# Performance work log

Hardware: AMD Instinct MI355X
Metric: run time of the kernel (lower is better)

Reference implementation:

```python
import jax, jax.numpy as jnp
import numpy as np

DIM = 192
D_STATE = 16
D_CONV = 4
EXPAND = 2
D_INNER = DIM * EXPAND          # 384
DT_RANK = (DIM + 15) // 16      # 12
B_SZ, H_SP, W_SP = 4, 64, 64


def setup_inputs() -> dict:
    key = jax.random.key(0)
    ks = jax.random.split(key, 8)
    f = jax.random.normal
    return {
        "x": f(ks[0], (B_SZ, DIM, H_SP, W_SP), jnp.float32),
        "ln_w": jnp.ones((DIM,), jnp.float32),
        "ln_b": jnp.zeros((DIM,), jnp.float32),
        "in_proj_w": f(ks[1], (2 * D_INNER, DIM), jnp.float32) * 0.02,
        "conv_w": f(ks[2], (D_INNER, D_CONV), jnp.float32) * 0.2,
        "conv_b": jnp.zeros((D_INNER,), jnp.float32),
        "x_proj_w": f(ks[3], (DT_RANK + 2 * D_STATE, D_INNER), jnp.float32) * 0.02,
        "dt_proj_w": f(ks[4], (D_INNER, DT_RANK), jnp.float32) * 0.1,
        "dt_proj_b": f(ks[5], (D_INNER,), jnp.float32) * 0.1,
        "A_log": jnp.log(jnp.broadcast_to(
            jnp.arange(1, D_STATE + 1, dtype=jnp.float32), (D_INNER, D_STATE))),
        "D": jnp.ones((D_INNER,), jnp.float32),
        "out_proj_w": f(ks[6], (DIM, D_INNER), jnp.float32) * 0.02,
    }


def _mamba_block(x, ln_w, ln_b, in_proj_w, conv_w, conv_b, x_proj_w,
                 dt_proj_w, dt_proj_b, A_log, D, out_proj_w):
    B, C, H, W = x.shape
    L = H * W
    # [B,C,H,W] -> [B,L,C]
    xf = x.transpose(0, 2, 3, 1).reshape(B, L, C)

    # LayerNorm
    mu = xf.mean(-1, keepdims=True)
    var = ((xf - mu) ** 2).mean(-1, keepdims=True)
    xn = (xf - mu) * jax.lax.rsqrt(var + 1e-5) * ln_w + ln_b

    # in_proj -> xm (ssm branch), z (gate branch)
    xz = xn @ in_proj_w.T                      # [B,L,2*Di]
    xm, z = jnp.split(xz, 2, axis=-1)

    # causal depthwise conv1d over sequence (pad left d_conv-1)
    xc = xm.transpose(0, 2, 1)                 # [B,Di,L]
    xc = jax.lax.conv_general_dilated(
        xc, conv_w[:, None, :], (1,), [(D_CONV - 1, 0)],
        dimension_numbers=("NCH", "OIH", "NCH"),
        feature_group_count=D_INNER)
    xc = xc + conv_b[None, :, None]
    xm = jax.nn.silu(xc.transpose(0, 2, 1))    # [B,L,Di]

    # x_proj -> dt, B, C (input-dependent SSM params)
    dbc = xm @ x_proj_w.T                      # [B,L,dt_rank+2N]
    dt, Bm, Cm = jnp.split(dbc, [DT_RANK, DT_RANK + D_STATE], axis=-1)
    dt = jax.nn.softplus(dt @ dt_proj_w.T + dt_proj_b)  # [B,L,Di]

    A = -jnp.exp(A_log)                        # [Di,N]

    def step(h, inp):
        xt, dtt, Bt, Ct = inp                  # [B,Di],[B,Di],[B,N],[B,N]
        dA = jnp.exp(dtt[..., None] * A)       # [B,Di,N]
        h = h * dA + (dtt * xt)[..., None] * Bt[:, None, :]
        y = jnp.einsum('bdn,bn->bd', h, Ct)
        return h, y

    h0 = jnp.zeros((B, D_INNER, D_STATE), xm.dtype)
    scan_in = (xm.transpose(1, 0, 2), dt.transpose(1, 0, 2),
               Bm.transpose(1, 0, 2), Cm.transpose(1, 0, 2))
    _, ys = jax.lax.scan(step, h0, scan_in)    # [L,B,Di]

    y = ys.transpose(1, 0, 2) + xm * D         # skip term D*x
    y = y * jax.nn.silu(z)                     # gate
    out = y @ out_proj_w.T                     # [B,L,C]

    out = xf + out                             # residual
    return out.reshape(B, H, W, C).transpose(0, 3, 1, 2)


def reference(x, ln_w, ln_b, in_proj_w, conv_w, conv_b, x_proj_w,
              dt_proj_w, dt_proj_b, A_log, D, out_proj_w):
    return _mamba_block(x, ln_w, ln_b, in_proj_w, conv_w, conv_b, x_proj_w,
                        dt_proj_w, dt_proj_b, A_log, D, out_proj_w)
```

## Files before the change

kernel.cpp:

```cpp
#include <hip/hip_runtime.h>
#include <hip/hip_bf16.h>
#include <cstdint>
#include <cmath>

#define DIMC   192
#define DSTATE 16
#define DCONV  4
#define DINNER 384
#define DTRANK 12
#define BSZ    4
#define HSP    64
#define WSP    64
#define LSEQ   4096
#define NTOK   (BSZ*LSEQ)
#define XPN    (DTRANK + 2*DSTATE)
#define XZW    (2*DINNER)
#define LC4    16
#define NCH4   (LSEQ/LC4)
#define NXP    448

typedef unsigned short ushortT;
using short8 = __attribute__((ext_vector_type(8))) short;
using f32x4  = __attribute__((ext_vector_type(4))) float;

__device__ __forceinline__ float bflo(unsigned u) { return __uint_as_float(u << 16); }
__device__ __forceinline__ float bfhi(unsigned u) { return __uint_as_float(u & 0xffff0000u); }
__device__ __forceinline__ float bf2f(ushortT u) { return __uint_as_float(((unsigned)u) << 16); }
__device__ __forceinline__ unsigned pkbf(float lo, float hi) {
  __hip_bfloat16 l = __float2bfloat16(lo), h = __float2bfloat16(hi);
  return (unsigned)*(ushortT*)&l | ((unsigned)*(ushortT*)&h << 16);
}
#define UNPK8(arr, base, v4)                                        \
  arr[base + 0] = bflo(v4.x); arr[base + 1] = bfhi(v4.x);           \
  arr[base + 2] = bflo(v4.y); arr[base + 3] = bfhi(v4.y);           \
  arr[base + 4] = bflo(v4.z); arr[base + 5] = bfhi(v4.z);           \
  arr[base + 6] = bflo(v4.w); arr[base + 7] = bfhi(v4.w);

__global__ __launch_bounds__(256) void wcvt_kernel(
    const float* __restrict__ w_in, const float* __restrict__ w_out,
    __hip_bfloat16* __restrict__ wbf) {
  int gid = blockIdx.x * 256 + threadIdx.x;
  float v = gid < 147456 ? w_in[gid] : w_out[gid - 147456];
  wbf[gid] = __float2bfloat16(v);
}

__global__ __launch_bounds__(256) void wcomb_kernel(
    const float* __restrict__ xpw, const float* __restrict__ dtw,
    __hip_bfloat16* __restrict__ wcb) {
  int gid = blockIdx.x * 256 + threadIdx.x;
  int dd = gid / 384, k = gid % 384;
  float v = 0.f;
  if (dd < 384) {
#pragma unroll
    for (int j = 0; j < 12; ++j) v = fmaf(dtw[dd * 12 + j], xpw[j * 384 + k], v);
  } else if (dd < 416) {
    v = xpw[(dd - 372) * 384 + k];
  }
  wcb[gid] = __float2bfloat16(v);
}

__global__ __launch_bounds__(512) void ln_kernel(
    const float* __restrict__ x, const float* __restrict__ ln_w,
    const float* __restrict__ ln_b, __hip_bfloat16* __restrict__ xn) {
  __shared__ float xs[DIMC][WSP + 1];
  __shared__ float mu_s[WSP], rs_s[WSP];
  int bh = blockIdx.x;
  int b = bh >> 6, h = bh & 63;
  int tid = threadIdx.x;
  const float* xb = x + (size_t)b * DIMC * LSEQ + (size_t)h * WSP;
  for (int e = tid; e < DIMC * WSP; e += 512) {
    int c = e >> 6, w = e & 63;
    xs[c][w] = xb[(size_t)c * LSEQ + w];
  }
  __syncthreads();
  {
    int w = tid >> 3, p = tid & 7;
    float s = 0.f, s2 = 0.f;
#pragma unroll
    for (int i = 0; i < 24; ++i) {
      float v = xs[p * 24 + i][w];
      s += v; s2 = fmaf(v, v, s2);
    }
    s  += __shfl_xor(s, 1);  s2 += __shfl_xor(s2, 1);
    s  += __shfl_xor(s, 2);  s2 += __shfl_xor(s2, 2);
    s  += __shfl_xor(s, 4);  s2 += __shfl_xor(s2, 4);
    if (p == 0) {
      float mu = s * (1.f / DIMC);
      float var = s2 * (1.f / DIMC) - mu * mu;
      mu_s[w] = mu;
      rs_s[w] = rsqrtf(var + 1e-5f);
    }
  }
  __syncthreads();
  __hip_bfloat16* xo = xn + (size_t)(b * LSEQ + h * WSP) * DIMC;
  for (int e = tid; e < DIMC * WSP; e += 512) {
    int w = e / DIMC, c = e % DIMC;
    xo[(size_t)w * DIMC + c] =
        __float2bfloat16((xs[c][w] - mu_s[w]) * rs_s[w] * ln_w[c] + ln_b[c]);
  }
}

template<int WM, int WN, int FM, int FN, int EPI>
__global__ __launch_bounds__(256) void gemm_bf16(
    const ushortT* __restrict__ A, const ushortT* __restrict__ B,
    void* __restrict__ Cv, void* __restrict__ Cv2,
    const ushortT* __restrict__ xm_aux, const float* __restrict__ bias384,
    const float* __restrict__ xres, int K, int Nreal, int ldc) {
  constexpr int BM = WM * FM * 16, BN = WN * FN * 16;
  __shared__ ushortT As[BM][72];
  __shared__ ushortT Bs[BN][72];
  int bm = blockIdx.x * BM, bn = blockIdx.y * BN;
  int tid = threadIdx.x, lane = tid & 63, w = tid >> 6;
  int wm = w / WN, wn = w % WN;
  int lm = lane & 15, lk = lane >> 4;
  const ushortT* Bb = B;
  size_t zoff = 0;
  if constexpr (EPI == 1) {
    size_t zb = blockIdx.z;
    Bb = B + zb * (size_t)LSEQ * K;
    zoff = zb * (size_t)DIMC * LSEQ;
  }
  f32x4 acc[FM][FN];
#pragma unroll
  for (int mi = 0; mi < FM; ++mi)
#pragma unroll
    for (int ni = 0; ni < FN; ++ni) acc[mi][ni] = (f32x4){0.f, 0.f, 0.f, 0.f};

  for (int k0 = 0; k0 < K; k0 += 64) {
    __syncthreads();
    for (int v = tid; v < BM * 8; v += 256) {
      int row = v >> 3, c8 = v & 7;
      *(uint4*)&As[row][c8 * 8] =
          *(const uint4*)(A + (size_t)(bm + row) * K + k0 + c8 * 8);
    }
    for (int v = tid; v < BN * 8; v += 256) {
      int row = v >> 3, c8 = v & 7;
      *(uint4*)&Bs[row][c8 * 8] =
          *(const uint4*)(Bb + (size_t)(bn + row) * K + k0 + c8 * 8);
    }
    __syncthreads();
#pragma unroll
    for (int ks = 0; ks < 2; ++ks) {
      short8 af[FM], bfr[FN];
#pragma unroll
      for (int mi = 0; mi < FM; ++mi)
        af[mi] = *(const short8*)&As[wm * FM * 16 + mi * 16 + lm][ks * 32 + lk * 8];
#pragma unroll
      for (int ni = 0; ni < FN; ++ni)
        bfr[ni] = *(const short8*)&Bs[wn * FN * 16 + ni * 16 + lm][ks * 32 + lk * 8];
#pragma unroll
      for (int mi = 0; mi < FM; ++mi)
#pragma unroll
        for (int ni = 0; ni < FN; ++ni)
          acc[mi][ni] = __builtin_amdgcn_mfma_f32_16x16x32_bf16(
              af[mi], bfr[ni], acc[mi][ni], 0, 0, 0);
    }
  }
#pragma unroll
  for (int mi = 0; mi < FM; ++mi) {
#pragma unroll
    for (int ni = 0; ni < FN; ++ni) {
      int ncol = bn + wn * FN * 16 + ni * 16 + lm;
#pragma unroll
      for (int r = 0; r < 4; ++r) {
        int m = bm + wm * FM * 16 + mi * 16 + lk * 4 + r;
        if constexpr (EPI == 1) {
          size_t aidx = zoff + (size_t)m * LSEQ + ncol;
          ((float*)Cv)[aidx] = xres[aidx] + acc[mi][ni][r];
        } else if constexpr (EPI == 2) {
          if (ncol < Nreal)
            ((__hip_bfloat16*)Cv)[(size_t)m * ldc + ncol] =
                __float2bfloat16(acc[mi][ni][r]);
        } else {
          if (ncol < 384) {
            float dtr = acc[mi][ni][r] + bias384[ncol];
            float dt = dtr > 15.f ? dtr : __logf(1.f + __expf(dtr));
            float xmv = bf2f(xm_aux[(size_t)m * DINNER + ncol]);
            ((unsigned*)Cv)[(size_t)m * DINNER + ncol] = pkbf(dt, xmv);
          } else if (ncol < 416) {
            __hip_bfloat16 bv = __float2bfloat16(acc[mi][ni][r]);
            ((ushortT*)Cv2)[(size_t)m * 48 + 16 + (ncol - 384)] = *(ushortT*)&bv;
          }
        }
      }
    }
  }
}

__global__ __launch_bounds__(256) void conv_silu_kernel(
    const __hip_bfloat16* __restrict__ xz, const float* __restrict__ conv_w,
    const float* __restrict__ conv_b, __hip_bfloat16* __restrict__ xmh) {
  int g8 = blockIdx.x * 256 + threadIdx.x;
  int d8 = g8 % 48;
  int tok = g8 / 48;
  int l = tok & (LSEQ - 1);
  int d0 = d8 * 8;
  const ushortT* base = (const ushortT*)xz + (size_t)tok * XZW + d0;
  uint4 r0, r1, r2, r3;
  r3 = *(const uint4*)(base);
  r2 = l >= 1 ? *(const uint4*)(base - XZW)     : (uint4){0, 0, 0, 0};
  r1 = l >= 2 ? *(const uint4*)(base - 2 * XZW) : (uint4){0, 0, 0, 0};
  r0 = l >= 3 ? *(const uint4*)(base - 3 * XZW) : (uint4){0, 0, 0, 0};
  float x0[8], x1[8], x2[8], x3[8];
  UNPK8(x0, 0, r0) UNPK8(x1, 0, r1) UNPK8(x2, 0, r2) UNPK8(x3, 0, r3)
  ushortT outv[8];
#pragma unroll
  for (int j = 0; j < 8; ++j) {
    const float4 w = *(const float4*)(conv_w + (d0 + j) * 4);
    float acc = conv_b[d0 + j];
    acc = fmaf(w.x, x0[j], acc);
    acc = fmaf(w.y, x1[j], acc);
    acc = fmaf(w.z, x2[j], acc);
    acc = fmaf(w.w, x3[j], acc);
    float s = acc / (1.f + __expf(-acc));
    __hip_bfloat16 sb = __float2bfloat16(s);
    outv[j] = *(ushortT*)&sb;
  }
  *(uint4*)((ushortT*)xmh + (size_t)tok * DINNER + d0) = *(uint4*)outv;
}

__global__ __launch_bounds__(384) void scan_part1(
    const unsigned* __restrict__ dxpk, const ushortT* __restrict__ dbc,
    const float* __restrict__ A_log, unsigned* __restrict__ hpk) {
  __shared__ ushortT dbc_s[16 * 48];
  int d = threadIdx.x, c = blockIdx.x, b = blockIdx.y;
  size_t rowbase = (size_t)b * LSEQ + (size_t)c * LC4;
  if (d < 96) {
    int row = d / 6, q = d % 6;
    ((uint4*)dbc_s)[d] = ((const uint4*)(dbc + (rowbase + row) * 48))[q];
  }
  float Ac2[16];
#pragma unroll
  for (int q = 0; q < 4; ++q) {
    float4 t4 = *(const float4*)(A_log + d * 16 + q * 4);
    Ac2[q * 4 + 0] = -__expf(t4.x) * 1.44269504f;
    Ac2[q * 4 + 1] = -__expf(t4.y) * 1.44269504f;
    Ac2[q * 4 + 2] = -__expf(t4.z) * 1.44269504f;
    Ac2[q * 4 + 3] = -__expf(t4.w) * 1.44269504f;
  }
  float h[16];
#pragma unroll
  for (int n = 0; n < 16; ++n) h[n] = 0.f;
  float sdt = 0.f;
  const unsigned* pkp = dxpk + rowbase * DINNER + d;
  __syncthreads();
#pragma unroll
  for (int t0 = 0; t0 < 16; t0 += 4) {
    unsigned pk[4];
#pragma unroll
    for (int j = 0; j < 4; ++j) pk[j] = pkp[(t0 + j) * DINNER];
#pragma unroll
    for (int j = 0; j < 4; ++j) {
      int t = t0 + j;
      float dtt = bflo(pk[j]), xmv = bfhi(pk[j]);
      sdt += dtt;
      float dx = dtt * xmv;
      const char* bb = (const char*)dbc_s + t * 96;
      uint4 B0 = *(const uint4*)(bb + 32);
      uint4 B1 = *(const uint4*)(bb + 48);
      float Bv[16];
      UNPK8(Bv, 0, B0)
      UNPK8(Bv, 8, B1)
#pragma unroll
      for (int n = 0; n < 16; ++n) {
        float a = __builtin_amdgcn_exp2f(dtt * Ac2[n]);
        h[n] = fmaf(h[n], a, dx * Bv[n]);
      }
    }
  }
  unsigned up[16];
#pragma unroll
  for (int n = 0; n < 16; ++n)
    up[n] = pkbf(h[n], __builtin_amdgcn_exp2f(Ac2[n] * sdt));
  uint4* hp4 = (uint4*)(hpk + (((size_t)b * NCH4 + c) * DINNER + d) * 16);
#pragma unroll
  for (int q = 0; q < 4; ++q) hp4[q] = *(uint4*)&up[q * 4];
}

__global__ __launch_bounds__(256) void scan_part2(
    const unsigned* __restrict__ hpk, ushortT* __restrict__ hinb) {
  int e = blockIdx.x * 256 + threadIdx.x;
  int b = blockIdx.y;
  float H = 0.f;
  size_t base = (size_t)b * NCH4 * (DINNER * DSTATE) + e;
#pragma unroll 16
  for (int c = 0; c < NCH4; ++c) {
    size_t idx = base + (size_t)c * (DINNER * DSTATE);
    unsigned w = hpk[idx];
    __hip_bfloat16 hb = __float2bfloat16(H);
    hinb[idx] = *(ushortT*)&hb;
    H = fmaf(bfhi(w), H, bflo(w));
  }
}

__global__ __launch_bounds__(384) void scan_part3(
    const unsigned* __restrict__ dxpk, const ushortT* __restrict__ dbc,
    const __hip_bfloat16* __restrict__ xz, const float* __restrict__ A_log,
    const float* __restrict__ Dvec, const ushortT* __restrict__ hinb,
    __hip_bfloat16* __restrict__ ybuf) {
  __shared__ ushortT dbc_s[16 * 48];
  int d = threadIdx.x, c = blockIdx.x, b = blockIdx.y;
  size_t rowbase = (size_t)b * LSEQ + (size_t)c * LC4;
  if (d < 96) {
    int row = d / 6, q = d % 6;
    ((uint4*)dbc_s)[d] = ((const uint4*)(dbc + (rowbase + row) * 48))[q];
  }
  float Ac2[16];
#pragma unroll
  for (int q = 0; q < 4; ++q) {
    float4 t4 = *(const float4*)(A_log + d * 16 + q * 4);
    Ac2[q * 4 + 0] = -__expf(t4.x) * 1.44269504f;
    Ac2[q * 4 + 1] = -__expf(t4.y) * 1.44269504f;
    Ac2[q * 4 + 2] = -__expf(t4.z) * 1.44269504f;
    Ac2[q * 4 + 3] = -__expf(t4.w) * 1.44269504f;
  }
  float h[16];
  {
    const uint4* hp = (const uint4*)(hinb + (((size_t)b * NCH4 + c) * DINNER + d) * 16);
    uint4 h0 = hp[0], h1 = hp[1];
    UNPK8(h, 0, h0)
    UNPK8(h, 8, h1)
  }
  float Dd = Dvec[d];
  const unsigned* pkp = dxpk + rowbase * DINNER + d;
  const ushortT* zp = (const ushortT*)xz + rowbase * XZW + DINNER + d;
  __hip_bfloat16* yp = ybuf + rowbase * DINNER + d;
  __syncthreads();
#pragma unroll
  for (int t0 = 0; t0 < 16; t0 += 4) {
    unsigned pk[4];
    ushortT zv4[4];
#pragma unroll
    for (int j = 0; j < 4; ++j) {
      pk[j] = pkp[(t0 + j) * DINNER];
      zv4[j] = zp[(t0 + j) * XZW];
    }
#pragma unroll
    for (int j = 0; j < 4; ++j) {
      int t = t0 + j;
      float dtt = bflo(pk[j]), xmv = bfhi(pk[j]);
      float dx = dtt * xmv;
      const char* bb = (const char*)dbc_s + t * 96;
      uint4 B0 = *(const uint4*)(bb + 32);
      uint4 B1 = *(const uint4*)(bb + 48);
      uint4 C0 = *(const uint4*)(bb + 64);
      uint4 C1 = *(const uint4*)(bb + 80);
      float Bv[16], Cw[16];
      UNPK8(Bv, 0, B0)
      UNPK8(Bv, 8, B1)
      UNPK8(Cw, 0, C0)
      UNPK8(Cw, 8, C1)
      float y0 = 0.f, y1 = 0.f, y2 = 0.f, y3 = 0.f;
#pragma unroll
      for (int n = 0; n < 16; n += 4) {
        float a0 = __builtin_amdgcn_exp2f(dtt * Ac2[n + 0]);
        float a1 = __builtin_amdgcn_exp2f(dtt * Ac2[n + 1]);
        float a2 = __builtin_amdgcn_exp2f(dtt * Ac2[n + 2]);
        float a3 = __builtin_amdgcn_exp2f(dtt * Ac2[n + 3]);
        h[n + 0] = fmaf(h[n + 0], a0, dx * Bv[n + 0]);
        h[n + 1] = fmaf(h[n + 1], a1, dx * Bv[n + 1]);
        h[n + 2] = fmaf(h[n + 2], a2, dx * Bv[n + 2]);
        h[n + 3] = fmaf(h[n + 3], a3, dx * Bv[n + 3]);
        y0 = fmaf(h[n + 0], Cw[n + 0], y0);
        y1 = fmaf(h[n + 1], Cw[n + 1], y1);
        y2 = fmaf(h[n + 2], Cw[n + 2], y2);
        y3 = fmaf(h[n + 3], Cw[n + 3], y3);
      }
      float yv = fmaf(xmv, Dd, (y0 + y1) + (y2 + y3));
      float zv = bf2f(zv4[j]);
      float gt = zv * __builtin_amdgcn_rcpf(
          1.f + __builtin_amdgcn_exp2f(zv * -1.44269504f));
      yp[(size_t)t * DINNER] = __float2bfloat16(yv * gt);
    }
  }
}

extern "C" void kernel_launch(void* const* d_in, const int* in_sizes, int n_in,
                              void* d_out, int out_size, void* d_ws, size_t ws_size,
                              hipStream_t stream) {
  const float* x        = (const float*)d_in[0];
  const float* ln_w     = (const float*)d_in[1];
  const float* ln_b     = (const float*)d_in[2];
  const float* in_proj  = (const float*)d_in[3];
  const float* conv_w   = (const float*)d_in[4];
  const float* conv_b   = (const float*)d_in[5];
  const float* x_proj   = (const float*)d_in[6];
  const float* dt_w     = (const float*)d_in[7];
  const float* dt_b     = (const float*)d_in[8];
  const float* A_log    = (const float*)d_in[9];
  const float* Dvec     = (const float*)d_in[10];
  const float* out_proj = (const float*)d_in[11];
  float* out = (float*)d_out;

  float* ws = (float*)d_ws;
  __hip_bfloat16* xzb  = (__hip_bfloat16*)ws;
  __hip_bfloat16* xmh  = (__hip_bfloat16*)(ws + 6291456);
  ushortT*        dbcb = (ushortT*)(ws + 9437184);
  unsigned*       dxpk = (unsigned*)(ws + 9830400);
  unsigned*       hpk  = (unsigned*)(ws + 16121856);
  ushortT*        hinb = (ushortT*)(ws + 22413312);
  __hip_bfloat16* ybuf = (__hip_bfloat16*)(ws + 25559040);
  __hip_bfloat16* xnbf = (__hip_bfloat16*)(ws + 28704768);
  __hip_bfloat16* wbf  = (__hip_bfloat16*)(ws + 30277632);
  __hip_bfloat16* wcb  = (__hip_bfloat16*)(ws + 30388224);

  const ushortT* win  = (const ushortT*)wbf;
  const ushortT* wout = (const ushortT*)(wbf + 147456);

  wcvt_kernel<<<864, 256, 0, stream>>>(in_proj, out_proj, wbf);
  wcomb_kernel<<<672, 256, 0, stream>>>(x_proj, dt_w, wcb);

  ln_kernel<<<BSZ * HSP, 512, 0, stream>>>(x, ln_w, ln_b, xnbf);

  gemm_bf16<2, 2, 4, 4, 2><<<dim3(NTOK / 128, XZW / 128), 256, 0, stream>>>(
      (const ushortT*)xnbf, win, xzb, nullptr, nullptr, nullptr, nullptr,
      DIMC, XZW, XZW);

  conv_silu_kernel<<<(NTOK * DINNER / 8) / 256, 256, 0, stream>>>(
      xzb, conv_w, conv_b, xmh);

  gemm_bf16<2, 2, 4, 2, 4><<<dim3(NTOK / 128, NXP / 64), 256, 0, stream>>>(
      (const ushortT*)xmh, (const ushortT*)wcb, dxpk, dbcb,
      (const ushortT*)xmh, dt_b, nullptr, DINNER, NXP, 0);

  scan_part1<<<dim3(NCH4, BSZ), 384, 0, stream>>>(dxpk, dbcb, A_log, hpk);
  scan_part2<<<dim3(DINNER * DSTATE / 256, BSZ), 256, 0, stream>>>(hpk, hinb);
  scan_part3<<<dim3(NCH4, BSZ), 384, 0, stream>>>(
      dxpk, dbcb, xzb, A_log, Dvec, hinb, ybuf);

  gemm_bf16<2, 2, 2, 4, 1><<<dim3(DIMC / 64, LSEQ / 128, BSZ), 256, 0, stream>>>(
      wout, (const ushortT*)ybuf, out, nullptr, nullptr, nullptr, x,
      DINNER, LSEQ, LSEQ);
}
```

Before: 174.7 us.

## Prefetch GEMM tiles in registers, stage out_proj epilogue, merge weight prep kernels

The GEMM now prefetches the next K-slice of A and B into registers while the current tile is being consumed from LDS, so global loads overlap with MFMA work. The out_proj epilogue is staged through LDS (reusing the tile buffer) so the residual read and the output write become coalesced float4 accesses. The two weight-preparation kernels are merged into one launch. The x_proj GEMM is padded to 512 columns and retiled to 128-wide blocks. The padding computes extra zero columns in exchange for fewer, larger blocks, and the register prefetch raises register pressure.

Measured after the change: 215.3 us. 1.23x slower.

```diff
diff --git a/kernel.cpp b/kernel.cpp
--- a/kernel.cpp
+++ b/kernel.cpp
@@ -13,11 +13,10 @@
 #define WSP    64
 #define LSEQ   4096
 #define NTOK   (BSZ*LSEQ)
-#define XPN    (DTRANK + 2*DSTATE)
 #define XZW    (2*DINNER)
 #define LC4    16
 #define NCH4   (LSEQ/LC4)
-#define NXP    448
+#define NXP    512
 
 typedef unsigned short ushortT;
 using short8 = __attribute__((ext_vector_type(8))) short;
@@ -36,27 +35,26 @@
   arr[base + 4] = bflo(v4.z); arr[base + 5] = bfhi(v4.z);           \
   arr[base + 6] = bflo(v4.w); arr[base + 7] = bfhi(v4.w);
 
-__global__ __launch_bounds__(256) void wcvt_kernel(
+__global__ __launch_bounds__(256) void prep_kernel(
     const float* __restrict__ w_in, const float* __restrict__ w_out,
-    __hip_bfloat16* __restrict__ wbf) {
+    const float* __restrict__ xpw, const float* __restrict__ dtw,
+    __hip_bfloat16* __restrict__ wbf, __hip_bfloat16* __restrict__ wcb) {
   int gid = blockIdx.x * 256 + threadIdx.x;
-  float v = gid < 147456 ? w_in[gid] : w_out[gid - 147456];
-  wbf[gid] = __float2bfloat16(v);
-}
-
-__global__ __launch_bounds__(256) void wcomb_kernel(
-    const float* __restrict__ xpw, const float* __restrict__ dtw,
-    __hip_bfloat16* __restrict__ wcb) {
-  int gid = blockIdx.x * 256 + threadIdx.x;
-  int dd = gid / 384, k = gid % 384;
-  float v = 0.f;
-  if (dd < 384) {
-#pragma unroll
-    for (int j = 0; j < 12; ++j) v = fmaf(dtw[dd * 12 + j], xpw[j * 384 + k], v);
-  } else if (dd < 416) {
-    v = xpw[(dd - 372) * 384 + k];
-  }
-  wcb[gid] = __float2bfloat16(v);
+  if (gid < 221184) {
+    float v = gid < 147456 ? w_in[gid] : w_out[gid - 147456];
+    wbf[gid] = __float2bfloat16(v);
+  } else {
+    int e = gid - 221184;
+    int dd = e / 384, k = e % 384;
+    float v = 0.f;
+    if (dd < 384) {
+#pragma unroll
+      for (int j = 0; j < 12; ++j) v = fmaf(dtw[dd * 12 + j], xpw[j * 384 + k], v);
+    } else if (dd < 416) {
+      v = xpw[(dd - 372) * 384 + k];
+    }
+    wcb[e] = __float2bfloat16(v);
+  }
 }
 
 __global__ __launch_bounds__(512) void ln_kernel(
@@ -107,8 +105,14 @@
     const ushortT* __restrict__ xm_aux, const float* __restrict__ bias384,
     const float* __restrict__ xres, int K, int Nreal, int ldc) {
   constexpr int BM = WM * FM * 16, BN = WN * FN * 16;
-  __shared__ ushortT As[BM][72];
-  __shared__ ushortT Bs[BN][72];
+  constexpr int AV = BM * 8 / 256;
+  constexpr int BV = BN * 8 / 256;
+  constexpr int SM_AB = (BM + BN) * 72 * 2;
+  constexpr int SM_CT = (EPI == 1) ? BM * (BN + 4) * 4 : 0;
+  constexpr int SMEM = SM_AB > SM_CT ? SM_AB : SM_CT;
+  __shared__ __align__(16) char smem[SMEM];
+  ushortT (*As)[72] = (ushortT(*)[72])smem;
+  ushortT (*Bs)[72] = (ushortT(*)[72])(smem + (size_t)BM * 72 * 2);
   int bm = blockIdx.x * BM, bn = blockIdx.y * BN;
   int tid = threadIdx.x, lane = tid & 63, w = tid >> 6;
   int wm = w / WN, wn = w % WN;
@@ -126,19 +130,43 @@
 #pragma unroll
     for (int ni = 0; ni < FN; ++ni) acc[mi][ni] = (f32x4){0.f, 0.f, 0.f, 0.f};
 
+  uint4 areg[AV], breg[BV];
+#pragma unroll
+  for (int i = 0; i < AV; ++i) {
+    int v = tid + i * 256, row = v >> 3, c8 = v & 7;
+    areg[i] = *(const uint4*)(A + (size_t)(bm + row) * K + c8 * 8);
+  }
+#pragma unroll
+  for (int i = 0; i < BV; ++i) {
+    int v = tid + i * 256, row = v >> 3, c8 = v & 7;
+    breg[i] = *(const uint4*)(Bb + (size_t)(bn + row) * K + c8 * 8);
+  }
+
   for (int k0 = 0; k0 < K; k0 += 64) {
     __syncthreads();
-    for (int v = tid; v < BM * 8; v += 256) {
-      int row = v >> 3, c8 = v & 7;
-      *(uint4*)&As[row][c8 * 8] =
-          *(const uint4*)(A + (size_t)(bm + row) * K + k0 + c8 * 8);
-    }
-    for (int v = tid; v < BN * 8; v += 256) {
-      int row = v >> 3, c8 = v & 7;
-      *(uint4*)&Bs[row][c8 * 8] =
-          *(const uint4*)(Bb + (size_t)(bn + row) * K + k0 + c8 * 8);
+#pragma unroll
+    for (int i = 0; i < AV; ++i) {
+      int v = tid + i * 256, row = v >> 3, c8 = v & 7;
+      *(uint4*)&As[row][c8 * 8] = areg[i];
+    }
+#pragma unroll
+    for (int i = 0; i < BV; ++i) {
+      int v = tid + i * 256, row = v >> 3, c8 = v & 7;
+      *(uint4*)&Bs[row][c8 * 8] = breg[i];
     }
     __syncthreads();
+    if (k0 + 64 < K) {
+#pragma unroll
+      for (int i = 0; i < AV; ++i) {
+        int v = tid + i * 256, row = v >> 3, c8 = v & 7;
+        areg[i] = *(const uint4*)(A + (size_t)(bm + row) * K + k0 + 64 + c8 * 8);
+      }
+#pragma unroll
+      for (int i = 0; i < BV; ++i) {
+        int v = tid + i * 256, row = v >> 3, c8 = v & 7;
+        breg[i] = *(const uint4*)(Bb + (size_t)(bn + row) * K + k0 + 64 + c8 * 8);
+      }
+    }
 #pragma unroll
     for (int ks = 0; ks < 2; ++ks) {
       short8 af[FM], bfr[FN];
@@ -156,30 +184,54 @@
               af[mi], bfr[ni], acc[mi][ni], 0, 0, 0);
     }
   }
-#pragma unroll
-  for (int mi = 0; mi < FM; ++mi) {
-#pragma unroll
-    for (int ni = 0; ni < FN; ++ni) {
-      int ncol = bn + wn * FN * 16 + ni * 16 + lm;
-#pragma unroll
-      for (int r = 0; r < 4; ++r) {
-        int m = bm + wm * FM * 16 + mi * 16 + lk * 4 + r;
-        if constexpr (EPI == 1) {
-          size_t aidx = zoff + (size_t)m * LSEQ + ncol;
-          ((float*)Cv)[aidx] = xres[aidx] + acc[mi][ni][r];
-        } else if constexpr (EPI == 2) {
-          if (ncol < Nreal)
-            ((__hip_bfloat16*)Cv)[(size_t)m * ldc + ncol] =
-                __float2bfloat16(acc[mi][ni][r]);
-        } else {
-          if (ncol < 384) {
-            float dtr = acc[mi][ni][r] + bias384[ncol];
-            float dt = dtr > 15.f ? dtr : __logf(1.f + __expf(dtr));
-            float xmv = bf2f(xm_aux[(size_t)m * DINNER + ncol]);
-            ((unsigned*)Cv)[(size_t)m * DINNER + ncol] = pkbf(dt, xmv);
-          } else if (ncol < 416) {
-            __hip_bfloat16 bv = __float2bfloat16(acc[mi][ni][r]);
-            ((ushortT*)Cv2)[(size_t)m * 48 + 16 + (ncol - 384)] = *(ushortT*)&bv;
+
+  if constexpr (EPI == 1) {
+    __syncthreads();
+    float (*Ct)[BN + 4] = (float(*)[BN + 4])smem;
+#pragma unroll
+    for (int mi = 0; mi < FM; ++mi)
+#pragma unroll
+      for (int ni = 0; ni < FN; ++ni)
+#pragma unroll
+        for (int r = 0; r < 4; ++r)
+          Ct[wm * FM * 16 + mi * 16 + lk * 4 + r][wn * FN * 16 + ni * 16 + lm] =
+              acc[mi][ni][r];
+    __syncthreads();
+    float* Cout = (float*)Cv;
+    for (int e = tid; e < BM * (BN / 4); e += 256) {
+      int row = e / (BN / 4), q = e % (BN / 4);
+      size_t gidx = zoff + (size_t)(bm + row) * LSEQ + bn + q * 4;
+      float4 rv = *(const float4*)(xres + gidx);
+      float4 o;
+      o.x = Ct[row][q * 4 + 0] + rv.x;
+      o.y = Ct[row][q * 4 + 1] + rv.y;
+      o.z = Ct[row][q * 4 + 2] + rv.z;
+      o.w = Ct[row][q * 4 + 3] + rv.w;
+      *(float4*)(Cout + gidx) = o;
+    }
+  } else {
+#pragma unroll
+    for (int mi = 0; mi < FM; ++mi) {
+#pragma unroll
+      for (int ni = 0; ni < FN; ++ni) {
+        int ncol = bn + wn * FN * 16 + ni * 16 + lm;
+#pragma unroll
+        for (int r = 0; r < 4; ++r) {
+          int m = bm + wm * FM * 16 + mi * 16 + lk * 4 + r;
+          if constexpr (EPI == 2) {
+            if (ncol < Nreal)
+              ((__hip_bfloat16*)Cv)[(size_t)m * ldc + ncol] =
+                  __float2bfloat16(acc[mi][ni][r]);
+          } else {
+            if (ncol < 384) {
+              float dtr = acc[mi][ni][r] + bias384[ncol];
+              float dt = dtr > 15.f ? dtr : __logf(1.f + __expf(dtr));
+              float xmv = bf2f(xm_aux[(size_t)m * DINNER + ncol]);
+              ((unsigned*)Cv)[(size_t)m * DINNER + ncol] = pkbf(dt, xmv);
+            } else if (ncol < 416) {
+              __hip_bfloat16 bv = __float2bfloat16(acc[mi][ni][r]);
+              ((ushortT*)Cv2)[(size_t)m * 48 + 16 + (ncol - 384)] = *(ushortT*)&bv;
+            }
           }
         }
       }
@@ -407,8 +459,7 @@
   const ushortT* win  = (const ushortT*)wbf;
   const ushortT* wout = (const ushortT*)(wbf + 147456);
 
-  wcvt_kernel<<<864, 256, 0, stream>>>(in_proj, out_proj, wbf);
-  wcomb_kernel<<<672, 256, 0, stream>>>(x_proj, dt_w, wcb);
+  prep_kernel<<<1632, 256, 0, stream>>>(in_proj, out_proj, x_proj, dt_w, wbf, wcb);
 
   ln_kernel<<<BSZ * HSP, 512, 0, stream>>>(x, ln_w, ln_b, xnbf);
 
@@ -419,7 +470,7 @@
   conv_silu_kernel<<<(NTOK * DINNER / 8) / 256, 256, 0, stream>>>(
       xzb, conv_w, conv_b, xmh);
 
-  gemm_bf16<2, 2, 4, 2, 4><<<dim3(NTOK / 128, NXP / 64), 256, 0, stream>>>(
+  gemm_bf16<2, 2, 4, 4, 4><<<dim3(NTOK / 128, NXP / 128), 256, 0, stream>>>(
       (const ushortT*)xmh, (const ushortT*)wcb, dxpk, dbcb,
       (const ushortT*)xmh, dt_b, nullptr, DINNER, NXP, 0);
 
```
